# Kernel optimization log

Hardware: AMD Instinct MI355X
Metric: run time of the kernel (lower is better)

Reference implementation:

```python
import jax, jax.numpy as jnp
import numpy as np

EPS = 1e-5
BLOCKS = 8

def _bn(x, g, b, m, v):
    # eval-mode BatchNorm1d over channel dim of [B, C, T]
    return g[:, None] * (x - m[:, None]) * jax.lax.rsqrt(v[:, None] + EPS) + b[:, None]

def _conv1x1(x, w):
    # x: [B, Cin, T], w: [Cout, Cin] -> [B, Cout, T]
    return jnp.einsum('bct,oc->bot', x, w)

def _dwconv(x, w, dil):
    # x: [B, C, T], w: [C, K] depthwise dilated conv, 'same' padding
    C, K = w.shape
    pad = dil * (K - 1) // 2
    return jax.lax.conv_general_dilated(
        x, w[:, None, :], window_strides=(1,), padding=[(pad, pad)],
        rhs_dilation=(dil,), dimension_numbers=('NCH', 'OIH', 'NCH'),
        feature_group_count=C)

def setup_inputs() -> dict:
    key = jax.random.key(0)
    ks = jax.random.split(key, 16)
    B, Cb, H, T, K = 16, 256, 512, 4096, 3
    d = {}
    d['x'] = jax.random.normal(ks[0], (B, Cb, T), jnp.float32)
    d['bn1_gamma'] = jax.random.uniform(ks[1], (BLOCKS, Cb), jnp.float32)
    d['bn1_beta'] = jax.random.normal(ks[2], (BLOCKS, Cb), jnp.float32)
    d['bn1_mean'] = jax.random.normal(ks[3], (BLOCKS, Cb), jnp.float32)
    d['bn1_var'] = jax.random.uniform(ks[4], (BLOCKS, Cb), jnp.float32)
    d['w1'] = jax.random.normal(ks[5], (BLOCKS, H, Cb), jnp.float32)
    d['bn2_gamma'] = jax.random.uniform(ks[6], (BLOCKS, H), jnp.float32)
    d['bn2_beta'] = jax.random.normal(ks[7], (BLOCKS, H), jnp.float32)
    d['bn2_mean'] = jax.random.normal(ks[8], (BLOCKS, H), jnp.float32)
    d['bn2_var'] = jax.random.uniform(ks[9], (BLOCKS, H), jnp.float32)
    d['dw_w'] = jax.random.normal(ks[10], (BLOCKS, H, K), jnp.float32)
    d['bn3_gamma'] = jax.random.uniform(ks[11], (BLOCKS, H), jnp.float32)
    d['bn3_beta'] = jax.random.normal(ks[12], (BLOCKS, H), jnp.float32)
    d['bn3_mean'] = jax.random.normal(ks[13], (BLOCKS, H), jnp.float32)
    d['bn3_var'] = jax.random.uniform(ks[14], (BLOCKS, H), jnp.float32)
    d['w2'] = jax.random.normal(ks[15], (BLOCKS, Cb, H), jnp.float32)
    return d

def reference(x, bn1_gamma, bn1_beta, bn1_mean, bn1_var, w1,
              bn2_gamma, bn2_beta, bn2_mean, bn2_var, dw_w,
              bn3_gamma, bn3_beta, bn3_mean, bn3_var, w2):
    sign = jnp.sign  # binary activation on inputs and weights
    resid = x
    for i in range(BLOCKS):
        dil = 2 ** i
        h = _bn(resid, bn1_gamma[i], bn1_beta[i], bn1_mean[i], bn1_var[i])
        h = _conv1x1(sign(h), sign(w1[i]))                 # 1x1, Cb -> H
        h = _bn(h, bn2_gamma[i], bn2_beta[i], bn2_mean[i], bn2_var[i])
        h = _dwconv(sign(h), sign(dw_w[i]), dil)           # depthwise dilated
        h = _bn(h, bn3_gamma[i], bn3_beta[i], bn3_mean[i], bn3_var[i])
        h = _conv1x1(sign(h), sign(w2[i]))                 # 1x1, H -> Cb
        resid = resid + h
    return resid
```

## Files before the change

### kernel.cpp

```cpp
#include <hip/hip_runtime.h>
#include <stdint.h>

namespace {
constexpr int Bn  = 16;
constexpr int Cc  = 256;
constexpr int Hn  = 512;
constexpr int Tn  = 4096;
constexpr int CWn = Cc / 32;
constexpr int HWn = Hn / 32;
constexpr int TWn = Tn / 32;
constexpr int TC  = 64;
constexpr float EPSf = 1e-5f;
}

typedef __attribute__((ext_vector_type(4)))  int i32x4;
typedef __attribute__((ext_vector_type(16))) int i32x16;

__global__ __launch_bounds__(256) void setup_kernel(
    const float* __restrict__ bn1g, const float* __restrict__ bn1b,
    const float* __restrict__ bn1m, const float* __restrict__ bn1v,
    const float* __restrict__ w1,
    const float* __restrict__ bn2g, const float* __restrict__ bn2b,
    const float* __restrict__ bn2m, const float* __restrict__ bn2v,
    const float* __restrict__ dww,
    const float* __restrict__ bn3g, const float* __restrict__ bn3b,
    const float* __restrict__ bn3m, const float* __restrict__ bn3v,
    const float* __restrict__ w2,
    float* __restrict__ thr1, float* __restrict__ thr2, float* __restrict__ thr3,
    uint32_t* __restrict__ dws, uint32_t* __restrict__ W1p,
    uint8_t* __restrict__ W1u, int* __restrict__ Sw1, int* __restrict__ T2i,
    uint8_t* __restrict__ W2uf, int* __restrict__ Sw2)
{
  const int idx = blockIdx.x * 256 + threadIdx.x;
  if (idx < 8 * Hn * CWn) {
    const int w = idx & (CWn - 1);
    const int h = idx >> 3;
    const float* src = w1 + (size_t)h * Cc + w * 32;
    uint32_t word = 0;
#pragma unroll
    for (int j = 0; j < 32; ++j) word |= (uint32_t)(src[j] > 0.f) << j;
    W1p[h * CWn + w] = word;
    atomicAdd(&Sw1[h], (int)__popc(word));
    uint32_t* dst = (uint32_t*)(W1u + (size_t)h * 256);
#pragma unroll
    for (int q = 0; q < 8; ++q) {
      const uint32_t dw = (((word >> (4 * q)) & 0xFu) * 0x00204081u) & 0x01010101u;
      const int off = (w * 32 + q * 4) ^ ((h & 15) << 4);
      dst[off >> 2] = dw;
    }
  } else {
    const int k = idx - 8 * Hn * CWn;
    const int w = k & (HWn - 1);
    const int c = k >> 4;
    const float* src = w2 + (size_t)c * Hn + w * 32;
    uint32_t word = 0;
#pragma unroll
    for (int j = 0; j < 32; ++j) word |= (uint32_t)(src[j] > 0.f) << j;
    atomicAdd(&Sw2[c], (int)__popc(word));
    const int blk = c >> 8, cl = c & 255;
    uint32_t* dst = (uint32_t*)(W2uf + (size_t)blk * 131072);
#pragma unroll
    for (int q = 0; q < 8; ++q) {
      const uint32_t dw = (((word >> (4 * q)) & 0xFu) * 0x00204081u) & 0x01010101u;
      dst[((w * 2 + (q >> 2)) * 256 + cl) * 4 + (q & 3)] = dw;
    }
  }
  if (idx < 8 * Cc)
    thr1[idx] = bn1m[idx] - bn1b[idx] * sqrtf(bn1v[idx] + EPSf) / bn1g[idx];
  if (idx < 8 * Hn) {
    const float th2 = bn2m[idx] - bn2b[idx] * sqrtf(bn2v[idx] + EPSf) / bn2g[idx];
    thr2[idx] = th2;
    int T;
    if (th2 >= 8.0e6f)       T =  (1 << 24);
    else if (th2 <= -8.0e6f) T = -(1 << 24);
    else if (th2 == th2)     T = (int)floorf(th2) + 1;
    else                     T =  (1 << 24);
    T2i[idx] = T;
    thr3[idx] = bn3m[idx] - bn3b[idx] * sqrtf(bn3v[idx] + EPSf) / bn3g[idx];
    uint32_t dw = 0;
    for (int k2 = 0; k2 < 3; ++k2) dw |= (uint32_t)(dww[(size_t)idx * 3 + k2] > 0.f) << k2;
    dws[idx] = dw;
  }
}

__global__ __launch_bounds__(256) void k1_pack(
    const float* __restrict__ resid, const float* __restrict__ thr1,
    uint32_t* __restrict__ Xp)
{
  const int idx = blockIdx.x * 256 + threadIdx.x;
  const int t  = idx & (Tn - 1);
  const int cw = (idx >> 12) & (CWn - 1);
  const int b  = idx >> 15;
  const float* r = resid + ((size_t)(b * Cc + cw * 32)) * Tn + t;
  uint32_t word = 0;
#pragma unroll
  for (int j = 0; j < 32; ++j)
    word |= (uint32_t)(r[(size_t)j * Tn] > thr1[cw * 32 + j]) << j;
  Xp[((size_t)b * CWn + cw) * Tn + t] = word;
}

__global__ __launch_bounds__(256) void k2_gemm1(
    const uint32_t* __restrict__ Xp, const uint32_t* __restrict__ W1p,
    const float* __restrict__ thr2, uint32_t* __restrict__ Y)
{
  const int bid  = blockIdx.x;
  const int tblk = bid & 15;
  const int og   = (bid >> 4) & 63;
  const int b    = bid >> 10;
  const int t    = tblk * 256 + threadIdx.x;
  const int o    = og * 8;

  const uint32_t* xrow = Xp + (size_t)b * CWn * Tn + t;
  const uint32_t* wrow = W1p + o * CWn;
  int acc[8] = {0, 0, 0, 0, 0, 0, 0, 0};
#pragma unroll
  for (int w = 0; w < CWn; ++w) {
    const uint32_t xw = xrow[(size_t)w * Tn];
#pragma unroll
    for (int r = 0; r < 8; ++r)
      acc[r] += __popc(xw ^ wrow[r * CWn + w]);
  }
  const int lane = threadIdx.x & 63;
#pragma unroll
  for (int r = 0; r < 8; ++r) {
    const float v = (float)(Cc - 2 * acc[r]);
    const uint64_t m = __ballot(v > thr2[o + r]);
    if ((lane & 31) == 0)
      Y[((size_t)b * TWn + (t >> 5)) * Hn + o + r] = (uint32_t)(m >> lane);
  }
}

__global__ __launch_bounds__(512) void k_iter(
    const uint32_t* __restrict__ Yin, const uint32_t* __restrict__ dws,
    const float* __restrict__ thr3,
    const uint8_t* __restrict__ W2uf, const int* __restrict__ Sw2_i,
    const float* __restrict__ rin, float* __restrict__ rout,
    const float* __restrict__ thr1n,
    const uint8_t* __restrict__ W1u_n, const int* __restrict__ Sw1_n,
    const int* __restrict__ T2i_n, uint32_t* __restrict__ Yout,
    int dil, int do_next)
{
  __shared__ __align__(16) uint8_t ZW[TC * 512];
  __shared__ __align__(16) uint8_t Xi8[TC * 256];
  __shared__ int   Tc[Hn];
  __shared__ float thr1L[Cc];
  __shared__ int   Sw2x2L[Cc];
  __shared__ int   Sx[TC], Sz[TC];

  const int chunk = blockIdx.x & (Tn / TC - 1);
  const int b     = blockIdx.x >> 6;
  const int tid   = threadIdx.x;
  const int lane  = tid & 63;
  const int wid   = __builtin_amdgcn_readfirstlane(tid >> 6);
  const int lh    = lane & 31;
  const int twL   = lane >> 5;
  const int tw0   = chunk * 2;

  if (tid < TC) { Sx[tid] = 0; Sz[tid] = 0; }
  if (tid < Cc) { thr1L[tid] = thr1n[tid]; Sw2x2L[tid] = 2 * Sw2_i[tid]; }
  __syncthreads();

#pragma unroll
  for (int task = 0; task < 2; ++task) {
    const int hw = wid * 2 + task;
    const int tw = tw0 + twL;
    const int ch = hw * 32 + lh;

    const uint32_t* yb = Yin + (size_t)b * TWn * Hn + ch;
    const uint32_t ycur = yb[(size_t)tw * Hn];
    uint32_t yl, yr, Vl, Vr;
    if (dil >= 32) {
      const int dw = dil >> 5;
      const bool lok = tw >= dw, rok = tw + dw < TWn;
      yl = lok ? yb[(size_t)(tw - dw) * Hn] : 0u;
      yr = rok ? yb[(size_t)(tw + dw) * Hn] : 0u;
      Vl = lok ? ~0u : 0u;
      Vr = rok ? ~0u : 0u;
    } else {
      const uint32_t yp = (tw > 0) ? yb[(size_t)(tw - 1) * Hn] : 0u;
      const uint32_t yn = (tw < TWn - 1) ? yb[(size_t)(tw + 1) * Hn] : 0u;
      yl = (ycur << dil) | ((tw > 0) ? (yp >> (32 - dil)) : 0u);
      yr = (ycur >> dil) | ((tw < TWn - 1) ? (yn << (32 - dil)) : 0u);
      Vl = (tw == 0) ? (~0u << dil) : ~0u;
      Vr = (tw == TWn - 1) ? (~0u >> dil) : ~0u;
    }
    const uint32_t d = dws[ch];
    const uint32_t a  = ((d & 1u) ? yl : ~yl) & Vl;
    const uint32_t bb = (d & 2u) ? ycur : ~ycur;
    const uint32_t c  = ((d & 4u) ? yr : ~yr) & Vr;

    const float thr = thr3[ch];
    const float v3 = (thr + 3.f) * 0.5f;
    const float v2 = (thr + 2.f) * 0.5f;
    const int K3 = (int)(v3 >= 0.f) + (int)(v3 >= 1.f) + (int)(v3 >= 2.f) + (int)(v3 >= 3.f);
    const int K2 = (int)(v2 >= 0.f) + (int)(v2 >= 1.f) + (int)(v2 >= 2.f);

    const uint32_t g1 = a | bb | c;
    const uint32_t g2 = (a & bb) | (c & (a | bb));
    const uint32_t g3 = a & bb & c;
    const uint32_t full = (K3 == 0) ? ~0u : (K3 == 1) ? g1 : (K3 == 2) ? g2
                        : (K3 == 3) ? g3 : 0u;
    const uint32_t lm = (K2 == 0) ? ~0u : (K2 == 1) ? (bb | c) : (K2 == 2) ? (bb & c) : 0u;
    const uint32_t rm = (K2 == 0) ? ~0u : (K2 == 1) ? (a | bb) : (K2 == 2) ? (a & bb) : 0u;

    uint32_t w = (Vl & Vr & full) | (~Vl & lm) | (~Vr & rm);

#pragma unroll
    for (int s = 16; s; s >>= 1) {
      const uint32_t m = 0xFFFFFFFFu / ((1u << s) + 1u);
      const uint32_t o = __shfl_xor(w, s, 64);
      w = ((lane & s) == 0) ? ((w & m) | ((o & m) << s))
                            : ((w & ~m) | ((o & ~m) >> s));
    }
    const int swzA = (lane & 15) << 4;
    uint32_t e[8];
#pragma unroll
    for (int q = 0; q < 8; ++q)
      e[q] = (((w >> (4 * q)) & 0xFu) * 0x00204081u) & 0x01010101u;
    i32x4 v0; v0[0] = e[0]; v0[1] = e[1]; v0[2] = e[2]; v0[3] = e[3];
    i32x4 v1; v1[0] = e[4]; v1[1] = e[5]; v1[2] = e[6]; v1[3] = e[7];
    *(i32x4*)&ZW[lane * 512 + ((hw * 32)      ^ swzA)] = v0;
    *(i32x4*)&ZW[lane * 512 + ((hw * 32 + 16) ^ swzA)] = v1;
    atomicAdd(&Sz[lane], (int)__popc(w));
  }
  __syncthreads();

  {
    const int mc   = wid;
    const int half = lane >> 5;
    const int lrow = mc * 32 + lh;
    const int t0   = chunk * TC;

    float rv0[16], rv1[16];
#pragma unroll
    for (int r = 0; r < 16; ++r) {
      const int cr = mc * 32 + (r & 3) + 8 * (r >> 2) + 4 * half;
      const float* rowp = rin + ((size_t)(b * Cc + cr)) * Tn + t0;
      rv0[r] = rowp[lh];
      rv1[r] = rowp[32 + lh];
    }

    const int swz0 = (lh & 15) << 4;
    i32x16 acc0 = {0,0,0,0, 0,0,0,0, 0,0,0,0, 0,0,0,0};
    i32x16 acc1 = {0,0,0,0, 0,0,0,0, 0,0,0,0, 0,0,0,0};
#pragma unroll
    for (int ks = 0; ks < 16; ++ks) {
      const int k0 = ks * 32 + half * 16;
      const i32x4 af  = *(const i32x4*)(W2uf + (((size_t)(ks * 2 + half) * 256 + lrow) * 16));
      const i32x4 bf0 = *(const i32x4*)&ZW[lh * 512 + (k0 ^ swz0)];
      const i32x4 bf1 = *(const i32x4*)&ZW[(32 + lh) * 512 + (k0 ^ swz0)];
      acc0 = __builtin_amdgcn_mfma_i32_32x32x32_i8(af, bf0, acc0, 0, 0, 0);
      acc1 = __builtin_amdgcn_mfma_i32_32x32x32_i8(af, bf1, acc1, 0, 0, 0);
    }

    const int Sz0 = 2 * Sz[lh], Sz1 = 2 * Sz[32 + lh];
    uint32_t dw0[4] = {0,0,0,0}, dw1[4] = {0,0,0,0};
#pragma unroll
    for (int r = 0; r < 16; ++r) {
      const int cr = mc * 32 + (r & 3) + 8 * (r >> 2) + 4 * half;
      const int sw2 = Sw2x2L[cr];
      const float th = thr1L[cr];
      float* orow = rout + ((size_t)(b * Cc + cr)) * Tn + t0;
      const float ro0 = rv0[r] + (float)((acc0[r] << 2) - Sz0 - sw2 + 512);
      const float ro1 = rv1[r] + (float)((acc1[r] << 2) - Sz1 - sw2 + 512);
      orow[lh]      = ro0;
      orow[32 + lh] = ro1;
      dw0[r >> 2] |= (uint32_t)(ro0 > th) << ((r & 3) * 8);
      dw1[r >> 2] |= (uint32_t)(ro1 > th) << ((r & 3) * 8);
    }
    int cnt0 = 0, cnt1 = 0;
#pragma unroll
    for (int g = 0; g < 4; ++g) {
      const int cb = mc * 32 + g * 8 + half * 4;
      *(uint32_t*)&Xi8[lh * 256 + (cb ^ swz0)]        = dw0[g];
      *(uint32_t*)&Xi8[(32 + lh) * 256 + (cb ^ swz0)] = dw1[g];
      cnt0 += __popc(dw0[g]); cnt1 += __popc(dw1[g]);
    }
    atomicAdd(&Sx[lh], cnt0);
    atomicAdd(&Sx[32 + lh], cnt1);
  }
  __syncthreads();

  if (do_next) {
    Tc[tid] = T2i_n[tid] + 2 * Sw1_n[tid] - 256;

    const int ntile = wid & 1;
    const int mloc  = wid >> 1;
    const int tloc  = ntile * 32 + (lane & 31);
    const int half  = lane >> 5;

    i32x4 bf[8];
#pragma unroll
    for (int ks = 0; ks < 8; ++ks) {
      const int koff = (ks * 32 + half * 16) ^ ((tloc & 15) << 4);
      bf[ks] = *(const i32x4*)&Xi8[tloc * 256 + koff];
    }
    const int Sxv2 = 2 * Sx[tloc];
    uint32_t* yo = Yout + ((size_t)b * TWn + (chunk * 2 + ntile)) * Hn;

#pragma unroll 1
    for (int msup = 0; msup < 4; ++msup) {
      const uint32_t* gsrc = (const uint32_t*)(W1u_n + msup * 32768);
      uint32_t* ldst = (uint32_t*)ZW;
      i32x4 stg[4];
#pragma unroll
      for (int s = 0; s < 4; ++s)
        stg[s] = *(const i32x4*)&gsrc[(s * 512 + tid) * 4];
#pragma unroll
      for (int s = 0; s < 4; ++s)
        *(i32x4*)&ldst[(s * 512 + tid) * 4] = stg[s];
      __syncthreads();

      const int lrow = mloc * 32 + (lane & 31);
      i32x16 acc = {0,0,0,0, 0,0,0,0, 0,0,0,0, 0,0,0,0};
#pragma unroll
      for (int ks = 0; ks < 8; ++ks) {
        const int aoff = (ks * 32 + half * 16) ^ ((lrow & 15) << 4);
        const i32x4 af = *(const i32x4*)&ZW[lrow * 256 + aoff];
        acc = __builtin_amdgcn_mfma_i32_32x32x32_i8(af, bf[ks], acc, 0, 0, 0);
      }

      const int obase = msup * 128 + mloc * 32;
#pragma unroll
      for (int r = 0; r < 16; ++r) {
        const int row = (r & 3) + 8 * (r >> 2) + 4 * half;
        const int o = obase + row;
        const uint64_t m = __ballot((acc[r] << 2) >= Tc[o] + Sxv2);
        if ((lane & 31) == 0) yo[o] = (uint32_t)(m >> lane);
      }
      __syncthreads();
    }
  }
}

extern "C" void kernel_launch(void* const* d_in, const int* in_sizes, int n_in,
                              void* d_out, int out_size, void* d_ws, size_t ws_size,
                              hipStream_t stream)
{
  const float* x     = (const float*)d_in[0];
  const float* bn1g  = (const float*)d_in[1];
  const float* bn1b  = (const float*)d_in[2];
  const float* bn1m  = (const float*)d_in[3];
  const float* bn1v  = (const float*)d_in[4];
  const float* w1    = (const float*)d_in[5];
  const float* bn2g  = (const float*)d_in[6];
  const float* bn2b  = (const float*)d_in[7];
  const float* bn2m  = (const float*)d_in[8];
  const float* bn2v  = (const float*)d_in[9];
  const float* dww   = (const float*)d_in[10];
  const float* bn3g  = (const float*)d_in[11];
  const float* bn3b  = (const float*)d_in[12];
  const float* bn3m  = (const float*)d_in[13];
  const float* bn3v  = (const float*)d_in[14];
  const float* w2    = (const float*)d_in[15];
  float* out = (float*)d_out;

  char* ws = (char*)d_ws;
  uint32_t* Xp  = (uint32_t*)(ws);
  uint32_t* Ya  = (uint32_t*)(ws + (2u  << 20));
  uint32_t* Yb  = (uint32_t*)(ws + (6u  << 20));
  uint32_t* W1p = (uint32_t*)(ws + (10u << 20));
  float*    thr1 = (float*)(ws + (10u << 20) + (256u << 10));
  float*    thr2 = thr1 + 8 * Cc;
  float*    thr3 = thr2 + 8 * Hn;
  uint32_t* dws  = (uint32_t*)(thr3 + 8 * Hn);
  uint8_t*  W1u  = (uint8_t*)(ws + (11u << 20));
  int*      Sw1  = (int*)(ws + (12u << 20));
  int*      Sw2  = (int*)(ws + (12u << 20) + (16u << 10));
  int*      T2i  = (int*)(ws + (12u << 20) + (24u << 10));
  uint8_t*  W2uf = (uint8_t*)(ws + (13u << 20));

  hipMemsetAsync(Sw1, 0, (24u << 10), stream);

  setup_kernel<<<256, 256, 0, stream>>>(bn1g, bn1b, bn1m, bn1v, w1,
                                        bn2g, bn2b, bn2m, bn2v, dww,
                                        bn3g, bn3b, bn3m, bn3v, w2,
                                        thr1, thr2, thr3, dws, W1p,
                                        W1u, Sw1, T2i, W2uf, Sw2);

  k1_pack <<<2048,  256, 0, stream>>>(x, thr1, Xp);
  k2_gemm1<<<16384, 256, 0, stream>>>(Xp, W1p, thr2, Ya);

  for (int i = 0; i < 8; ++i) {
    const float* rin = (i == 0) ? x : out;
    const int inext = (i < 7) ? i + 1 : 7;
    const uint32_t* Yin  = (i & 1) ? Yb : Ya;
    uint32_t*       Yout = (i & 1) ? Ya : Yb;
    k_iter<<<1024, 512, 0, stream>>>(Yin, dws + i * Hn, thr3 + i * Hn,
                                     W2uf + (size_t)i * 131072, Sw2 + i * Cc,
                                     rin, out,
                                     thr1 + inext * Cc,
                                     W1u + (size_t)inext * Hn * 256,
                                     Sw1 + inext * Hn, T2i + inext * Hn,
                                     Yout, 1 << i, (i < 7) ? 1 : 0);
  }
}
```

Before: 376.8 us.

## Load W1 MFMA fragments directly from global in fragment layout, drop LDS staging

Setup now writes the next block's binarized W1 weights in an MFMA-fragment-ordered layout, the same way W2 is already stored. The fused iteration kernel then loads A fragments straight from global memory into registers instead of staging each 128-row slab through shared memory, which removes four block-wide barriers per iteration. W2 fragment loads are batched eight at a time ahead of the MFMAs, and the per-lane Sz atomics are merged into one per thread. The Tc threshold setup moves to the kernel prologue. The cost is higher register pressure and more global and L2 traffic in exchange for fewer barriers.

```diff
diff --git a/kernel.cpp b/kernel.cpp
--- a/kernel.cpp
+++ b/kernel.cpp
@@ -28,7 +28,7 @@
     const float* __restrict__ w2,
     float* __restrict__ thr1, float* __restrict__ thr2, float* __restrict__ thr3,
     uint32_t* __restrict__ dws, uint32_t* __restrict__ W1p,
-    uint8_t* __restrict__ W1u, int* __restrict__ Sw1, int* __restrict__ T2i,
+    uint8_t* __restrict__ W1f, int* __restrict__ Sw1, int* __restrict__ T2i,
     uint8_t* __restrict__ W2uf, int* __restrict__ Sw2)
 {
   const int idx = blockIdx.x * 256 + threadIdx.x;
@@ -41,12 +41,12 @@
     for (int j = 0; j < 32; ++j) word |= (uint32_t)(src[j] > 0.f) << j;
     W1p[h * CWn + w] = word;
     atomicAdd(&Sw1[h], (int)__popc(word));
-    uint32_t* dst = (uint32_t*)(W1u + (size_t)h * 256);
+    const int blk = h >> 9, hl = h & 511;
+    uint32_t* dst = (uint32_t*)(W1f + (size_t)blk * 131072);
 #pragma unroll
     for (int q = 0; q < 8; ++q) {
       const uint32_t dw = (((word >> (4 * q)) & 0xFu) * 0x00204081u) & 0x01010101u;
-      const int off = (w * 32 + q * 4) ^ ((h & 15) << 4);
-      dst[off >> 2] = dw;
+      dst[((w * 2 + (q >> 2)) * 512 + hl) * 4 + (q & 3)] = dw;
     }
   } else {
     const int k = idx - 8 * Hn * CWn;
@@ -136,11 +136,11 @@
     const uint8_t* __restrict__ W2uf, const int* __restrict__ Sw2_i,
     const float* __restrict__ rin, float* __restrict__ rout,
     const float* __restrict__ thr1n,
-    const uint8_t* __restrict__ W1u_n, const int* __restrict__ Sw1_n,
+    const uint8_t* __restrict__ W1f_n, const int* __restrict__ Sw1_n,
     const int* __restrict__ T2i_n, uint32_t* __restrict__ Yout,
     int dil, int do_next)
 {
-  __shared__ __align__(16) uint8_t ZW[TC * 512];
+  __shared__ __align__(16) uint8_t Zi8[TC * 512];
   __shared__ __align__(16) uint8_t Xi8[TC * 256];
   __shared__ int   Tc[Hn];
   __shared__ float thr1L[Cc];
@@ -158,8 +158,10 @@
 
   if (tid < TC) { Sx[tid] = 0; Sz[tid] = 0; }
   if (tid < Cc) { thr1L[tid] = thr1n[tid]; Sw2x2L[tid] = 2 * Sw2_i[tid]; }
+  Tc[tid] = T2i_n[tid] + 2 * Sw1_n[tid] - 256;
   __syncthreads();
 
+  int zcnt = 0;
 #pragma unroll
   for (int task = 0; task < 2; ++task) {
     const int hw = wid * 2 + task;
@@ -219,10 +221,11 @@
       e[q] = (((w >> (4 * q)) & 0xFu) * 0x00204081u) & 0x01010101u;
     i32x4 v0; v0[0] = e[0]; v0[1] = e[1]; v0[2] = e[2]; v0[3] = e[3];
     i32x4 v1; v1[0] = e[4]; v1[1] = e[5]; v1[2] = e[6]; v1[3] = e[7];
-    *(i32x4*)&ZW[lane * 512 + ((hw * 32)      ^ swzA)] = v0;
-    *(i32x4*)&ZW[lane * 512 + ((hw * 32 + 16) ^ swzA)] = v1;
-    atomicAdd(&Sz[lane], (int)__popc(w));
-  }
+    *(i32x4*)&Zi8[lane * 512 + ((hw * 32)      ^ swzA)] = v0;
+    *(i32x4*)&Zi8[lane * 512 + ((hw * 32 + 16) ^ swzA)] = v1;
+    zcnt += (int)__popc(w);
+  }
+  atomicAdd(&Sz[lane], zcnt);
   __syncthreads();
 
   {
@@ -244,13 +247,22 @@
     i32x16 acc0 = {0,0,0,0, 0,0,0,0, 0,0,0,0, 0,0,0,0};
     i32x16 acc1 = {0,0,0,0, 0,0,0,0, 0,0,0,0, 0,0,0,0};
 #pragma unroll
-    for (int ks = 0; ks < 16; ++ks) {
-      const int k0 = ks * 32 + half * 16;
-      const i32x4 af  = *(const i32x4*)(W2uf + (((size_t)(ks * 2 + half) * 256 + lrow) * 16));
-      const i32x4 bf0 = *(const i32x4*)&ZW[lh * 512 + (k0 ^ swz0)];
-      const i32x4 bf1 = *(const i32x4*)&ZW[(32 + lh) * 512 + (k0 ^ swz0)];
-      acc0 = __builtin_amdgcn_mfma_i32_32x32x32_i8(af, bf0, acc0, 0, 0, 0);
-      acc1 = __builtin_amdgcn_mfma_i32_32x32x32_i8(af, bf1, acc1, 0, 0, 0);
+    for (int kg = 0; kg < 2; ++kg) {
+      i32x4 afv[8];
+#pragma unroll
+      for (int kk = 0; kk < 8; ++kk) {
+        const int ks = kg * 8 + kk;
+        afv[kk] = *(const i32x4*)(W2uf + (((size_t)(ks * 2 + half) * 256 + lrow) * 16));
+      }
+#pragma unroll
+      for (int kk = 0; kk < 8; ++kk) {
+        const int ks = kg * 8 + kk;
+        const int k0 = ks * 32 + half * 16;
+        const i32x4 bf0 = *(const i32x4*)&Zi8[lh * 512 + (k0 ^ swz0)];
+        const i32x4 bf1 = *(const i32x4*)&Zi8[(32 + lh) * 512 + (k0 ^ swz0)];
+        acc0 = __builtin_amdgcn_mfma_i32_32x32x32_i8(afv[kk], bf0, acc0, 0, 0, 0);
+        acc1 = __builtin_amdgcn_mfma_i32_32x32x32_i8(afv[kk], bf1, acc1, 0, 0, 0);
+      }
     }
 
     const int Sz0 = 2 * Sz[lh], Sz1 = 2 * Sz[32 + lh];
@@ -282,11 +294,9 @@
   __syncthreads();
 
   if (do_next) {
-    Tc[tid] = T2i_n[tid] + 2 * Sw1_n[tid] - 256;
-
     const int ntile = wid & 1;
     const int mloc  = wid >> 1;
-    const int tloc  = ntile * 32 + (lane & 31);
+    const int tloc  = ntile * 32 + lh;
     const int half  = lane >> 5;
 
     i32x4 bf[8];
@@ -300,35 +310,24 @@
 
 #pragma unroll 1
     for (int msup = 0; msup < 4; ++msup) {
-      const uint32_t* gsrc = (const uint32_t*)(W1u_n + msup * 32768);
-      uint32_t* ldst = (uint32_t*)ZW;
-      i32x4 stg[4];
-#pragma unroll
-      for (int s = 0; s < 4; ++s)
-        stg[s] = *(const i32x4*)&gsrc[(s * 512 + tid) * 4];
-#pragma unroll
-      for (int s = 0; s < 4; ++s)
-        *(i32x4*)&ldst[(s * 512 + tid) * 4] = stg[s];
-      __syncthreads();
-
-      const int lrow = mloc * 32 + (lane & 31);
+      const int row = msup * 128 + mloc * 32 + lh;
+      i32x4 afv[8];
+#pragma unroll
+      for (int ks = 0; ks < 8; ++ks)
+        afv[ks] = *(const i32x4*)(W1f_n + (((size_t)(ks * 2 + half) * 512 + row) * 16));
       i32x16 acc = {0,0,0,0, 0,0,0,0, 0,0,0,0, 0,0,0,0};
 #pragma unroll
-      for (int ks = 0; ks < 8; ++ks) {
-        const int aoff = (ks * 32 + half * 16) ^ ((lrow & 15) << 4);
-        const i32x4 af = *(const i32x4*)&ZW[lrow * 256 + aoff];
-        acc = __builtin_amdgcn_mfma_i32_32x32x32_i8(af, bf[ks], acc, 0, 0, 0);
-      }
+      for (int ks = 0; ks < 8; ++ks)
+        acc = __builtin_amdgcn_mfma_i32_32x32x32_i8(afv[ks], bf[ks], acc, 0, 0, 0);
 
       const int obase = msup * 128 + mloc * 32;
 #pragma unroll
       for (int r = 0; r < 16; ++r) {
-        const int row = (r & 3) + 8 * (r >> 2) + 4 * half;
-        const int o = obase + row;
+        const int orow = (r & 3) + 8 * (r >> 2) + 4 * half;
+        const int o = obase + orow;
         const uint64_t m = __ballot((acc[r] << 2) >= Tc[o] + Sxv2);
         if ((lane & 31) == 0) yo[o] = (uint32_t)(m >> lane);
       }
-      __syncthreads();
     }
   }
 }
@@ -364,7 +363,7 @@
   float*    thr2 = thr1 + 8 * Cc;
   float*    thr3 = thr2 + 8 * Hn;
   uint32_t* dws  = (uint32_t*)(thr3 + 8 * Hn);
-  uint8_t*  W1u  = (uint8_t*)(ws + (11u << 20));
+  uint8_t*  W1f  = (uint8_t*)(ws + (11u << 20));
   int*      Sw1  = (int*)(ws + (12u << 20));
   int*      Sw2  = (int*)(ws + (12u << 20) + (16u << 10));
   int*      T2i  = (int*)(ws + (12u << 20) + (24u << 10));
@@ -376,7 +375,7 @@
                                         bn2g, bn2b, bn2m, bn2v, dww,
                                         bn3g, bn3b, bn3m, bn3v, w2,
                                         thr1, thr2, thr3, dws, W1p,
-                                        W1u, Sw1, T2i, W2uf, Sw2);
+                                        W1f, Sw1, T2i, W2uf, Sw2);
 
   k1_pack <<<2048,  256, 0, stream>>>(x, thr1, Xp);
   k2_gemm1<<<16384, 256, 0, stream>>>(Xp, W1p, thr2, Ya);
@@ -390,7 +389,7 @@
                                      W2uf + (size_t)i * 131072, Sw2 + i * Cc,
                                      rin, out,
                                      thr1 + inext * Cc,
-                                     W1u + (size_t)inext * Hn * 256,
+                                     W1f + (size_t)inext * 131072,
                                      Sw1 + inext * Hn, T2i + inext * Hn,
                                      Yout, 1 << i, (i < 7) ? 1 : 0);
   }
```

Measured after the change: 355.8 us. 5.6% less time.
